# Performance work log

Measured on AMD Instinct MI355X. Metric: run time of the kernel, lower is better.

## Reference

```python
import jax, jax.numpy as jnp
import numpy as np

B, S, E, H = 8, 2048, 512, 8
D = E // H  # head_dim = 64


def setup_inputs() -> dict:
    key0 = jax.random.key(0)
    ks = jax.random.split(key0, 12)
    scale = 1.0 / np.sqrt(E)
    return {
        "value": jax.random.normal(ks[0], (B, S, E), jnp.float32),
        "key": jax.random.normal(ks[1], (B, S, E), jnp.float32),
        "query": jax.random.normal(ks[2], (B, S, E), jnp.float32),
        "mask": jax.random.randint(ks[3], (B, 1, 1, S), 0, 2, jnp.int32),
        "wq": jax.random.normal(ks[4], (E, E), jnp.float32) * scale,
        "bq": jnp.zeros((E,), jnp.float32),
        "wk": jax.random.normal(ks[5], (E, E), jnp.float32) * scale,
        "bk": jnp.zeros((E,), jnp.float32),
        "wv": jax.random.normal(ks[6], (E, E), jnp.float32) * scale,
        "bv": jnp.zeros((E,), jnp.float32),
        "wo": jax.random.normal(ks[7], (E, E), jnp.float32) * scale,
        "bo": jnp.zeros((E,), jnp.float32),
    }


def reference(value, key, query, mask, wq, bq, wk, bk, wv, bv, wo, bo):
    b, s, e = query.shape
    # projections
    q = (query @ wq + bq).reshape(b, s, H, D)  # (B,S,H,D)
    k = (key @ wk + bk).reshape(b, s, H, D)
    v = (value @ wv + bv).reshape(b, s, H, D)
    # scaled dot-product logits: (B,H,Sq,Sk)
    logits = jnp.einsum("bqhd,bkhd->bhqk", q, k) / jnp.sqrt(jnp.asarray(D, q.dtype))
    logits = logits + mask.astype(logits.dtype) * -1e9  # mask==1 -> blocked
    attn = jax.nn.softmax(logits, axis=-1)
    out = jnp.einsum("bhqk,bkhd->bqhd", attn, v).reshape(b, s, e)
    return out @ wo + bo
```

## Files before the change

kernel.cpp:

```cpp
#include <hip/hip_runtime.h>

#define Bz 8
#define Sz 2048
#define Ez 512
#define Hz 8
#define Dz 64

typedef _Float16 f16;
typedef __attribute__((ext_vector_type(2))) _Float16 f16x2;
typedef __attribute__((ext_vector_type(8))) _Float16 f16x8;
typedef __attribute__((ext_vector_type(4))) float f32x4;

#define LOG2E 1.44269504f

__device__ __forceinline__ void async16(const void* g, void* l) {
    __builtin_amdgcn_global_load_lds(
        (const __attribute__((address_space(1))) unsigned int*)g,
        (__attribute__((address_space(3))) unsigned int*)l, 16, 0, 0);
}

__device__ __forceinline__ f16x2 pkrtz(float a, float b) {
    return __builtin_bit_cast(f16x2, __builtin_amdgcn_cvt_pkrtz(a, b));
}

__device__ __forceinline__ int swz(int row) {
    return (row & 7) ^ ((2 * ((row >> 3) & 3)) & 7);
}

__global__ __launch_bounds__(256)
void cast_kernel(const float* __restrict__ q, const float* __restrict__ k,
                 const float* __restrict__ v, const int* __restrict__ mask,
                 f16* __restrict__ qa, f16* __restrict__ ka, f16* __restrict__ va,
                 int* __restrict__ rnk, int* __restrict__ slen)
{
    const int z = blockIdx.y;
    const int tid = threadIdx.x;
    if (z == 3) {
        const int b = blockIdx.x;
        if (b >= Bz) return;
        __shared__ int sc2[2][256];
        const int* mp = mask + (size_t)b * Sz;
        int m[8], c = 0;
        #pragma unroll
        for (int j = 0; j < 8; ++j) { m[j] = mp[tid*8 + j]; c += (m[j] == 0); }
        sc2[0][tid] = c;
        __syncthreads();
        int src = 0;
        #pragma unroll
        for (int s = 1; s < 256; s <<= 1) {
            int vv = sc2[src][tid] + ((tid >= s) ? sc2[src][tid - s] : 0);
            sc2[src ^ 1][tid] = vv;
            src ^= 1;
            __syncthreads();
        }
        int incl = sc2[src][tid];
        int base = incl - c;
        if (tid == 255) slen[b] = incl;
        int kk = base;
        int r8[8];
        #pragma unroll
        for (int j = 0; j < 8; ++j) {
            r8[j] = (m[j] == 0) ? kk : -1;
            kk += (m[j] == 0);
        }
        #pragma unroll
        for (int j = 0; j < 8; ++j) rnk[(size_t)b * Sz + tid*8 + j] = r8[j];
        return;
    }
    const int i = blockIdx.x * 256 + tid;
    const float* src = (z == 0) ? q : (z == 1) ? k : v;
    f16* dst = (z == 0) ? qa : (z == 1) ? ka : va;
    float4 x = *(const float4*)&src[(size_t)i * 4];
    f16x2 h0 = pkrtz(x.x, x.y), h1 = pkrtz(x.z, x.w);
    f16 h[4] = {h0[0], h0[1], h1[0], h1[1]};
    *(uint2*)&dst[(size_t)i * 4] = *(uint2*)h;
}

__global__ __launch_bounds__(256)
void prep_w(const float* __restrict__ W0, const float* __restrict__ W1,
            const float* __restrict__ W2, const float* __restrict__ W3,
            f16* __restrict__ T0, f16* __restrict__ T1,
            f16* __restrict__ T2, f16* __restrict__ T3)
{
    __shared__ float S[64][68];
    const float* W = (blockIdx.z==0)?W0:(blockIdx.z==1)?W1:(blockIdx.z==2)?W2:W3;
    f16*         T = (blockIdx.z==0)?T0:(blockIdx.z==1)?T1:(blockIdx.z==2)?T2:T3;
    const float sc = (blockIdx.z == 0) ? 0.125f * LOG2E : 1.0f;
    const int k0 = blockIdx.x * 64, n0 = blockIdx.y * 64;
    const int tid = threadIdx.x;
    {
        int kr = tid >> 4, nc = (tid & 15) * 4;
        #pragma unroll
        for (int i = 0; i < 4; ++i) {
            float4 w4 = *(const float4*)&W[(size_t)(k0 + kr + i*16) * Ez + n0 + nc];
            S[kr + i*16][nc+0] = w4.x; S[kr + i*16][nc+1] = w4.y;
            S[kr + i*16][nc+2] = w4.z; S[kr + i*16][nc+3] = w4.w;
        }
    }
    __syncthreads();
    {
        int n = tid >> 2, kq = tid & 3;
        f16 h[16];
        #pragma unroll
        for (int j = 0; j < 16; ++j) h[j] = (f16)(S[kq*16 + j][n] * sc);
        f16* dst = &T[(size_t)(n0 + n) * Ez + k0 + kq*16];
        *(uint4*)&dst[0] = *(uint4*)&h[0];
        *(uint4*)&dst[8] = *(uint4*)&h[8];
    }
}

__global__ __launch_bounds__(256)
void compact_v(const f16* __restrict__ vp, const int* __restrict__ slen,
               f16* __restrict__ vt)
{
    const int ct = blockIdx.x, h = blockIdx.y, b = blockIdx.z;
    const int sl = slen[b];
    if (ct * 64 >= sl && !(ct == 0 && sl == 0)) return;
    __shared__ f16 S[64 * 72];
    const int tid = threadIdx.x;
    {
        int r = tid >> 2, ch = tid & 3;
        int j = ct * 64 + r;
        uint4 v0 = {0,0,0,0}, v1 = {0,0,0,0};
        if (j < sl) {
            const f16* srcp = vp + (((size_t)b * Hz + h) * Sz + j) * Dz + ch * 16;
            v0 = *(const uint4*)&srcp[0];
            v1 = *(const uint4*)&srcp[8];
        }
        *(uint4*)&S[r*72 + ch*16]     = v0;
        *(uint4*)&S[r*72 + ch*16 + 8] = v1;
    }
    __syncthreads();
    {
        int d = tid >> 2, kq = tid & 3;
        f16 hh[16];
        #pragma unroll
        for (int j = 0; j < 16; ++j) hh[j] = S[(kq*16 + j)*72 + d];
        f16* dst = vt + (((size_t)b * Hz + h) * Dz + d) * Sz + ct*64 + kq*16;
        *(uint4*)&dst[0] = *(uint4*)&hh[0];
        *(uint4*)&dst[8] = *(uint4*)&hh[8];
    }
}

__global__ __launch_bounds__(256, 4)
void proj_gemm(const f16* __restrict__ qa, const f16* __restrict__ ka,
               const f16* __restrict__ va,
               const f16* __restrict__ wtq, const f16* __restrict__ wtk,
               const f16* __restrict__ wtv,
               const float* __restrict__ bqp, const float* __restrict__ bkp,
               const float* __restrict__ bvp, const int* __restrict__ rnk,
               f16* __restrict__ qp, f16* __restrict__ kp, f16* __restrict__ vp)
{
    __shared__ __align__(16) char lds[32768];
    const int z = blockIdx.z;
    const f16* A  = (z==0)?qa:(z==1)?ka:va;
    const f16* Wt = (z==0)?wtq:(z==1)?wtk:wtv;
    const float* bias = (z==0)?bqp:(z==1)?bkp:bvp;
    f16* C16 = (z==0)?qp:(z==1)?kp:vp;
    const float bscale = (z==0) ? 0.125f*LOG2E : 1.0f;

    const int tid  = threadIdx.x;
    const int lane = tid & 63, w = tid >> 6;
    const int col  = lane & 15, quad = lane >> 4;
    const int wm = w & 1, wn = w >> 1;
    const int m0 = blockIdx.x * 128, n0 = blockIdx.y * 128;
    const int srow = lane >> 2, schunk = lane & 3;

    f32x4 acc[4][4];
    #pragma unroll
    for (int i = 0; i < 4; ++i)
        #pragma unroll
        for (int j = 0; j < 4; ++j) acc[i][j] = (f32x4){0.f,0.f,0.f,0.f};

    auto issue = [&](int t, int buf) {
        f16* As = (f16*)(lds + buf * 16384);
        f16* Ws = As + 4096;
        #pragma unroll
        for (int i = 0; i < 2; ++i) {
            int row = w*32 + i*16 + srow;
            int cl = schunk ^ ((row >> 1) & 3);
            async16(&A[(size_t)(m0 + row) * Ez + t*32 + cl*8],  &As[row*32 + schunk*8]);
            async16(&Wt[(size_t)(n0 + row) * Ez + t*32 + cl*8], &Ws[row*32 + schunk*8]);
        }
    };

    issue(0, 0);
    const int xrc = (col >> 1) & 3;

    for (int t = 0; t < 16; ++t) {
        const int cur = t & 1;
        __syncthreads();
        if (t < 15) issue(t + 1, cur ^ 1);
        f16* As = (f16*)(lds + cur * 16384);
        f16* Ws = As + 4096;
        f16x8 af[4];
        #pragma unroll
        for (int mi = 0; mi < 4; ++mi)
            af[mi] = *(const f16x8*)&As[(wm*64 + mi*16 + col)*32 + ((quad ^ xrc)*8)];
        #pragma unroll
        for (int ni = 0; ni < 4; ++ni) {
            f16x8 wf = *(const f16x8*)&Ws[(wn*64 + ni*16 + col)*32 + ((quad ^ xrc)*8)];
            #pragma unroll
            for (int mi = 0; mi < 4; ++mi)
                acc[mi][ni] = __builtin_amdgcn_mfma_f32_16x16x32_f16(af[mi], wf, acc[mi][ni], 0,0,0);
        }
    }

    const int rw = tid >> 1, half = tid & 1;
    const int m = m0 + rw, b = m >> 11, s = m & (Sz-1);
    int rowout = s;
    bool dostore = true;
    if (z != 0) {
        int rk = rnk[(size_t)b * Sz + s];
        dostore = (rk >= 0);
        rowout = rk;
    }

    f16* Tr = (f16*)lds;
    #pragma unroll
    for (int p = 0; p < 2; ++p) {
        __syncthreads();
        if (wn == p) {
            #pragma unroll
            for (int ni = 0; ni < 4; ++ni) {
                float bv = bias[n0 + p*64 + ni*16 + col] * bscale;
                #pragma unroll
                for (int mi = 0; mi < 4; ++mi)
                    #pragma unroll
                    for (int rr = 0; rr < 4; ++rr) {
                        int ml = wm*64 + mi*16 + quad*4 + rr;
                        Tr[ml*72 + ni*16 + col] = (f16)(acc[mi][ni][rr] + bv);
                    }
            }
        }
        __syncthreads();
        if (dostore) {
            int hh = (n0 >> 6) + p;
            f16* dst = &C16[(((size_t)b*Hz + hh)*Sz + rowout)*Dz + half*32];
            const f16* srcp = &Tr[rw*72 + half*32];
            #pragma unroll
            for (int j = 0; j < 4; ++j)
                *(uint4*)&dst[j*8] = *(const uint4*)&srcp[j*8];
        }
    }
}

__global__ __launch_bounds__(256, 4)
void out_gemm(const f16* __restrict__ A, const f16* __restrict__ Wt,
              const float* __restrict__ bias, float* __restrict__ Cf)
{
    __shared__ __align__(16) char lds[32768];
    const int tid  = threadIdx.x;
    const int lane = tid & 63, w = tid >> 6;
    const int col  = lane & 15, quad = lane >> 4;
    const int wm = w & 1, wn = w >> 1;
    const int m0 = blockIdx.x * 128, n0 = blockIdx.y * 128;
    const int srow = lane >> 2, schunk = lane & 3;

    f32x4 acc[4][4];
    #pragma unroll
    for (int i = 0; i < 4; ++i)
        #pragma unroll
        for (int j = 0; j < 4; ++j) acc[i][j] = (f32x4){0.f,0.f,0.f,0.f};

    auto issue = [&](int t, int buf) {
        f16* As = (f16*)(lds + buf * 16384);
        f16* Ws = As + 4096;
        #pragma unroll
        for (int i = 0; i < 2; ++i) {
            int row = w*32 + i*16 + srow;
            int cl = schunk ^ ((row >> 1) & 3);
            async16(&A[(size_t)(m0 + row) * Ez + t*32 + cl*8],  &As[row*32 + schunk*8]);
            async16(&Wt[(size_t)(n0 + row) * Ez + t*32 + cl*8], &Ws[row*32 + schunk*8]);
        }
    };

    issue(0, 0);
    const int xrc = (col >> 1) & 3;

    for (int t = 0; t < 16; ++t) {
        const int cur = t & 1;
        __syncthreads();
        if (t < 15) issue(t + 1, cur ^ 1);
        f16* As = (f16*)(lds + cur * 16384);
        f16* Ws = As + 4096;
        f16x8 af[4];
        #pragma unroll
        for (int mi = 0; mi < 4; ++mi)
            af[mi] = *(const f16x8*)&As[(wm*64 + mi*16 + col)*32 + ((quad ^ xrc)*8)];
        #pragma unroll
        for (int ni = 0; ni < 4; ++ni) {
            f16x8 wf = *(const f16x8*)&Ws[(wn*64 + ni*16 + col)*32 + ((quad ^ xrc)*8)];
            #pragma unroll
            for (int mi = 0; mi < 4; ++mi)
                acc[mi][ni] = __builtin_amdgcn_mfma_f32_16x16x32_f16(af[mi], wf, acc[mi][ni], 0,0,0);
        }
    }

    #pragma unroll
    for (int ni = 0; ni < 4; ++ni) {
        int n = n0 + wn*64 + ni*16 + col;
        float bv = bias[n];
        #pragma unroll
        for (int mi = 0; mi < 4; ++mi)
            #pragma unroll
            for (int rr = 0; rr < 4; ++rr) {
                int m = m0 + wm*64 + mi*16 + quad*4 + rr;
                Cf[(size_t)m * Ez + n] = acc[mi][ni][rr] + bv;
            }
    }
}

__global__ __launch_bounds__(256, 4)
void attn_f16(const f16* __restrict__ Q, const f16* __restrict__ K,
              const f16* __restrict__ VT, const int* __restrict__ slen,
              f16* __restrict__ O)
{
    __shared__ __align__(16) f16 KS[2][64*64];
    __shared__ __align__(16) f16 VS[2][64*64];

    const int tid  = threadIdx.x;
    const int lane = tid & 63, w = tid >> 6;
    const int col  = lane & 15, quad = lane >> 4;

    const int blk = blockIdx.x;
    const int xcd = blk & 7, slot = blk >> 3;
    const int bh = xcd + 8 * (slot >> 4);
    const int qb = slot & 15;
    const int b = bh >> 3, h = bh & 7;

    const int sl = slen[b];
    int nt = (sl + 63) >> 6;
    if (nt < 1) nt = 1;

    const int q0 = qb * 128 + w * 32;

    f16x8 qf[2][2];
    #pragma unroll
    for (int qt = 0; qt < 2; ++qt)
        #pragma unroll
        for (int ks = 0; ks < 2; ++ks)
            qf[qt][ks] = *(const f16x8*)&Q[((size_t)bh*Sz + q0 + qt*16 + col)*Dz + ks*32 + quad*8];

    const f16* Kp = K + (size_t)bh * Sz * Dz;
    const f16* Vp = VT + (size_t)bh * Dz * Sz;

    const int srow = lane >> 3, sch = lane & 7;
    const int row0 = w*16 + srow, row1 = row0 + 8;
    const int cl0 = sch ^ swz(row0), cl1 = sch ^ swz(row1);

    int keyrow[4], gk[4];
    #pragma unroll
    for (int kc = 0; kc < 4; ++kc) {
        keyrow[kc] = 32*(kc>>1) + 8*(col>>2) + 4*(kc&1) + (col&3);
        gk[kc] = swz(keyrow[kc]);
    }

    f32x4 oacc[2][4];
    #pragma unroll
    for (int qt = 0; qt < 2; ++qt)
        #pragma unroll
        for (int dc = 0; dc < 4; ++dc) oacc[qt][dc] = (f32x4){0.f,0.f,0.f,0.f};
    const f32x4 zero4 = (f32x4){0.f, 0.f, 0.f, 0.f};
    f32x4 lacc[2] = {(f32x4){0.f,0.f,0.f,0.f}, (f32x4){0.f,0.f,0.f,0.f}};
    f16x8 one8;
    #pragma unroll
    for (int i = 0; i < 8; ++i) one8[i] = (f16)1.0f;

    auto issue = [&](int t, int buf) {
        async16(&Kp[(size_t)(t*64 + row0)*Dz + cl0*8], &KS[buf][row0*64 + sch*8]);
        async16(&Vp[(size_t)row0*Sz + t*64 + cl0*8],   &VS[buf][row0*64 + sch*8]);
        async16(&Kp[(size_t)(t*64 + row1)*Dz + cl1*8], &KS[buf][row1*64 + sch*8]);
        async16(&Vp[(size_t)row1*Sz + t*64 + cl1*8],   &VS[buf][row1*64 + sch*8]);
    };

    issue(0, 0);

    for (int t = 0; t < nt; ++t) {
        const int cur = t & 1;
        __syncthreads();
        if (t + 1 < nt) issue(t + 1, cur ^ 1);

        f32x4 sc[2][4];
        __builtin_amdgcn_s_setprio(1);
        #pragma unroll
        for (int kc = 0; kc < 4; ++kc) {
            f16x8 kf0 = *(const f16x8*)&KS[cur][keyrow[kc]*64 + ((quad ^ gk[kc])*8)];
            f16x8 kf1 = *(const f16x8*)&KS[cur][keyrow[kc]*64 + (((4 + quad) ^ gk[kc])*8)];
            sc[0][kc] = __builtin_amdgcn_mfma_f32_16x16x32_f16(kf0, qf[0][0], zero4, 0,0,0);
            sc[1][kc] = __builtin_amdgcn_mfma_f32_16x16x32_f16(kf0, qf[1][0], zero4, 0,0,0);
            sc[0][kc] = __builtin_amdgcn_mfma_f32_16x16x32_f16(kf1, qf[0][1], sc[0][kc], 0,0,0);
            sc[1][kc] = __builtin_amdgcn_mfma_f32_16x16x32_f16(kf1, qf[1][1], sc[1][kc], 0,0,0);
        }
        __builtin_amdgcn_s_setprio(0);

        const bool last = (t == nt - 1);
        union { f16x2 h2[4]; f16x8 h8; } ph[2][2];
        #pragma unroll
        for (int qt = 0; qt < 2; ++qt) {
            #pragma unroll
            for (int kg = 0; kg < 2; ++kg) {
                float e0 = __builtin_amdgcn_exp2f(sc[qt][2*kg][0]);
                float e1 = __builtin_amdgcn_exp2f(sc[qt][2*kg][1]);
                float e2 = __builtin_amdgcn_exp2f(sc[qt][2*kg][2]);
                float e3 = __builtin_amdgcn_exp2f(sc[qt][2*kg][3]);
                float e4 = __builtin_amdgcn_exp2f(sc[qt][2*kg+1][0]);
                float e5 = __builtin_amdgcn_exp2f(sc[qt][2*kg+1][1]);
                float e6 = __builtin_amdgcn_exp2f(sc[qt][2*kg+1][2]);
                float e7 = __builtin_amdgcn_exp2f(sc[qt][2*kg+1][3]);
                if (last) {
                    int rem = sl - t*64 - 32*kg - 8*quad;
                    e0 = (rem > 0) ? e0 : 0.f; e1 = (rem > 1) ? e1 : 0.f;
                    e2 = (rem > 2) ? e2 : 0.f; e3 = (rem > 3) ? e3 : 0.f;
                    e4 = (rem > 4) ? e4 : 0.f; e5 = (rem > 5) ? e5 : 0.f;
                    e6 = (rem > 6) ? e6 : 0.f; e7 = (rem > 7) ? e7 : 0.f;
                }
                ph[qt][kg].h2[0] = pkrtz(e0, e1);
                ph[qt][kg].h2[1] = pkrtz(e2, e3);
                ph[qt][kg].h2[2] = pkrtz(e4, e5);
                ph[qt][kg].h2[3] = pkrtz(e6, e7);
            }
        }

        __builtin_amdgcn_s_setprio(1);
        lacc[0] = __builtin_amdgcn_mfma_f32_16x16x32_f16(one8, ph[0][0].h8, lacc[0], 0,0,0);
        lacc[1] = __builtin_amdgcn_mfma_f32_16x16x32_f16(one8, ph[1][0].h8, lacc[1], 0,0,0);
        lacc[0] = __builtin_amdgcn_mfma_f32_16x16x32_f16(one8, ph[0][1].h8, lacc[0], 0,0,0);
        lacc[1] = __builtin_amdgcn_mfma_f32_16x16x32_f16(one8, ph[1][1].h8, lacc[1], 0,0,0);
        #pragma unroll
        for (int dc = 0; dc < 4; ++dc) {
            const int d = dc*16 + col;
            const int gd = swz(d);
            #pragma unroll
            for (int kg = 0; kg < 2; ++kg) {
                f16x8 vf = *(const f16x8*)&VS[cur][d*64 + (((kg*4 + quad) ^ gd)*8)];
                oacc[0][dc] = __builtin_amdgcn_mfma_f32_16x16x32_f16(vf, ph[0][kg].h8, oacc[0][dc], 0,0,0);
                oacc[1][dc] = __builtin_amdgcn_mfma_f32_16x16x32_f16(vf, ph[1][kg].h8, oacc[1][dc], 0,0,0);
            }
        }
        __builtin_amdgcn_s_setprio(0);
    }

    float inv[2];
    inv[0] = 1.0f / lacc[0][0];
    inv[1] = 1.0f / lacc[1][0];
    #pragma unroll
    for (int qt = 0; qt < 2; ++qt) {
        const int q = q0 + qt*16 + col;
        f16* op = &O[((size_t)b*Sz + q)*Ez + h*Dz];
        #pragma unroll
        for (int dc = 0; dc < 4; ++dc) {
            f16 ov[4] = {(f16)(oacc[qt][dc][0]*inv[qt]), (f16)(oacc[qt][dc][1]*inv[qt]),
                         (f16)(oacc[qt][dc][2]*inv[qt]), (f16)(oacc[qt][dc][3]*inv[qt])};
            *(uint2*)&op[dc*16 + quad*4] = *(uint2*)ov;
        }
    }
}

extern "C" void kernel_launch(void* const* d_in, const int* in_sizes, int n_in,
                              void* d_out, int out_size, void* d_ws, size_t ws_size,
                              hipStream_t stream)
{
    const float* value = (const float*)d_in[0];
    const float* key   = (const float*)d_in[1];
    const float* query = (const float*)d_in[2];
    const int*   mask  = (const int*)d_in[3];
    const float* wq = (const float*)d_in[4];
    const float* bq = (const float*)d_in[5];
    const float* wk = (const float*)d_in[6];
    const float* bk = (const float*)d_in[7];
    const float* wv = (const float*)d_in[8];
    const float* bv = (const float*)d_in[9];
    const float* wo = (const float*)d_in[10];
    const float* bo = (const float*)d_in[11];
    float* out = (float*)d_out;

    const size_t nW   = (size_t)Ez * Ez;
    const size_t nAct = (size_t)Bz * Sz * Ez;
    f16* wtq = (f16*)d_ws;
    f16* wtk = wtq + nW;
    f16* wtv = wtk + nW;
    f16* wto = wtv + nW;
    f16* qa  = wto + nW;
    f16* ka  = qa + nAct;
    f16* va  = ka + nAct;
    f16* qp  = va + nAct;
    f16* kp  = qp + nAct;
    f16* vp  = kp + nAct;
    f16* vt  = vp + nAct;
    f16* o16 = vt + nAct;
    int* rnkp = (int*)(o16 + nAct);
    int* slenp = rnkp + Bz * Sz;

    cast_kernel<<<dim3(8192, 4), 256, 0, stream>>>(query, key, value, mask,
                                                   qa, ka, va, rnkp, slenp);
    prep_w<<<dim3(8, 8, 4), 256, 0, stream>>>(wq, wk, wv, wo, wtq, wtk, wtv, wto);

    proj_gemm<<<dim3(128, 4, 3), 256, 0, stream>>>(qa, ka, va, wtq, wtk, wtv,
                                                   bq, bk, bv, rnkp, qp, kp, vp);

    compact_v<<<dim3(32, Hz, Bz), 256, 0, stream>>>(vp, slenp, vt);

    attn_f16<<<1024, 256, 0, stream>>>(qp, kp, vt, slenp, o16);

    out_gemm<<<dim3(128, 4), 256, 0, stream>>>(o16, wto, bo, out);
}
```

Before: 273.3 us.

## Fuse V compaction and transpose into projection GEMM epilogue

Removes the separate compact_v kernel. The V projection epilogue now scatters unmasked rows straight into the transposed, compacted vt layout, using an LDS rank-to-row map and a per-tile minimum rank. The tail padding up to a multiple of 64 is zeroed in the mask-scan block of cast_kernel. This saves one launch and one full round trip of V through memory, but the transposed stores are 2-byte strided writes, which may coalesce poorly.

Result: no change. 278.0 us (+1.7%).

```diff
diff --git a/kernel.cpp b/kernel.cpp
--- a/kernel.cpp
+++ b/kernel.cpp
@@ -31,7 +31,7 @@
 void cast_kernel(const float* __restrict__ q, const float* __restrict__ k,
                  const float* __restrict__ v, const int* __restrict__ mask,
                  f16* __restrict__ qa, f16* __restrict__ ka, f16* __restrict__ va,
-                 int* __restrict__ rnk, int* __restrict__ slen)
+                 int* __restrict__ rnk, int* __restrict__ slen, f16* __restrict__ vt)
 {
     const int z = blockIdx.y;
     const int tid = threadIdx.x;
@@ -39,6 +39,7 @@
         const int b = blockIdx.x;
         if (b >= Bz) return;
         __shared__ int sc2[2][256];
+        __shared__ int ssl;
         const int* mp = mask + (size_t)b * Sz;
         int m[8], c = 0;
         #pragma unroll
@@ -55,7 +56,7 @@
         }
         int incl = sc2[src][tid];
         int base = incl - c;
-        if (tid == 255) slen[b] = incl;
+        if (tid == 255) { slen[b] = incl; ssl = incl; }
         int kk = base;
         int r8[8];
         #pragma unroll
@@ -65,6 +66,15 @@
         }
         #pragma unroll
         for (int j = 0; j < 8; ++j) rnk[(size_t)b * Sz + tid*8 + j] = r8[j];
+        __syncthreads();
+        const int sl2 = ssl;
+        const int pad = (sl2 + 63) & ~63;
+        if (pad > sl2) {
+            for (int pr = tid; pr < Hz * Dz; pr += 256) {
+                f16* dst = vt + ((size_t)b * Hz * Dz + pr) * Sz;
+                for (int j = sl2; j < pad; ++j) dst[j] = (f16)0.f;
+            }
+        }
         return;
     }
     const int i = blockIdx.x * 256 + tid;
@@ -109,39 +119,6 @@
     }
 }
 
-__global__ __launch_bounds__(256)
-void compact_v(const f16* __restrict__ vp, const int* __restrict__ slen,
-               f16* __restrict__ vt)
-{
-    const int ct = blockIdx.x, h = blockIdx.y, b = blockIdx.z;
-    const int sl = slen[b];
-    if (ct * 64 >= sl && !(ct == 0 && sl == 0)) return;
-    __shared__ f16 S[64 * 72];
-    const int tid = threadIdx.x;
-    {
-        int r = tid >> 2, ch = tid & 3;
-        int j = ct * 64 + r;
-        uint4 v0 = {0,0,0,0}, v1 = {0,0,0,0};
-        if (j < sl) {
-            const f16* srcp = vp + (((size_t)b * Hz + h) * Sz + j) * Dz + ch * 16;
-            v0 = *(const uint4*)&srcp[0];
-            v1 = *(const uint4*)&srcp[8];
-        }
-        *(uint4*)&S[r*72 + ch*16]     = v0;
-        *(uint4*)&S[r*72 + ch*16 + 8] = v1;
-    }
-    __syncthreads();
-    {
-        int d = tid >> 2, kq = tid & 3;
-        f16 hh[16];
-        #pragma unroll
-        for (int j = 0; j < 16; ++j) hh[j] = S[(kq*16 + j)*72 + d];
-        f16* dst = vt + (((size_t)b * Hz + h) * Dz + d) * Sz + ct*64 + kq*16;
-        *(uint4*)&dst[0] = *(uint4*)&hh[0];
-        *(uint4*)&dst[8] = *(uint4*)&hh[8];
-    }
-}
-
 __global__ __launch_bounds__(256, 4)
 void proj_gemm(const f16* __restrict__ qa, const f16* __restrict__ ka,
                const f16* __restrict__ va,
@@ -149,14 +126,13 @@
                const f16* __restrict__ wtv,
                const float* __restrict__ bqp, const float* __restrict__ bkp,
                const float* __restrict__ bvp, const int* __restrict__ rnk,
-               f16* __restrict__ qp, f16* __restrict__ kp, f16* __restrict__ vp)
+               f16* __restrict__ qp, f16* __restrict__ kp, f16* __restrict__ vt)
 {
     __shared__ __align__(16) char lds[32768];
     const int z = blockIdx.z;
     const f16* A  = (z==0)?qa:(z==1)?ka:va;
     const f16* Wt = (z==0)?wtq:(z==1)?wtk:wtv;
     const float* bias = (z==0)?bqp:(z==1)?bkp:bvp;
-    f16* C16 = (z==0)?qp:(z==1)?kp:vp;
     const float bscale = (z==0) ? 0.125f*LOG2E : 1.0f;
 
     const int tid  = threadIdx.x;
@@ -206,12 +182,37 @@
         }
     }
 
+    const int bb = m0 >> 11;
+    const int TS = (z == 2) ? 73 : 72;
+
+    int* rks  = (int*)(lds + 20480);
+    int* clp  = (int*)(lds + 22528);
+    int* sr0p = (int*)(lds + 24576);
+    int r0v = 0x7fffffff;
+    if (z == 2) {
+        __syncthreads();
+        if (tid == 0) sr0p[0] = 0x7fffffff;
+        if (tid < 128) clp[tid] = -1;
+        __syncthreads();
+        if (tid < 128) {
+            int rb = rnk[(size_t)bb * Sz + ((m0 + tid) & (Sz - 1))];
+            rks[tid] = rb;
+            if (rb >= 0) atomicMin(sr0p, rb);
+        }
+        __syncthreads();
+        r0v = sr0p[0];
+        if (tid < 128) {
+            int rb = rks[tid];
+            if (rb >= 0) clp[rb - r0v] = tid;
+        }
+    }
+
     const int rw = tid >> 1, half = tid & 1;
-    const int m = m0 + rw, b = m >> 11, s = m & (Sz-1);
+    const int s = (m0 + rw) & (Sz - 1);
     int rowout = s;
     bool dostore = true;
-    if (z != 0) {
-        int rk = rnk[(size_t)b * Sz + s];
+    if (z == 1) {
+        int rk = rnk[(size_t)bb * Sz + s];
         dostore = (rk >= 0);
         rowout = rk;
     }
@@ -229,18 +230,34 @@
                     #pragma unroll
                     for (int rr = 0; rr < 4; ++rr) {
                         int ml = wm*64 + mi*16 + quad*4 + rr;
-                        Tr[ml*72 + ni*16 + col] = (f16)(acc[mi][ni][rr] + bv);
+                        Tr[ml*TS + ni*16 + col] = (f16)(acc[mi][ni][rr] + bv);
                     }
             }
         }
         __syncthreads();
-        if (dostore) {
-            int hh = (n0 >> 6) + p;
-            f16* dst = &C16[(((size_t)b*Hz + hh)*Sz + rowout)*Dz + half*32];
-            const f16* srcp = &Tr[rw*72 + half*32];
-            #pragma unroll
-            for (int j = 0; j < 4; ++j)
-                *(uint4*)&dst[j*8] = *(const uint4*)&srcp[j*8];
+        const int hh = (n0 >> 6) + p;
+        if (z != 2) {
+            if (dostore) {
+                f16* C16 = (z == 0) ? qp : kp;
+                f16* dst = &C16[(((size_t)bb*Hz + hh)*Sz + rowout)*Dz + half*32];
+                const f16* srcp = &Tr[rw*TS + half*32];
+                #pragma unroll
+                for (int j = 0; j < 4; ++j)
+                    *(uint4*)&dst[j*8] = *(const uint4*)&srcp[j*8];
+            }
+        } else if (r0v != 0x7fffffff) {
+            const int jlane = tid & 63, dgrp = tid >> 6;
+            #pragma unroll
+            for (int dd = 0; dd < 16; ++dd) {
+                const int d = dgrp * 16 + dd;
+                f16* dstb = vt + (((size_t)bb * Hz + hh) * Dz + d) * Sz + r0v;
+                #pragma unroll
+                for (int jh = 0; jh < 2; ++jh) {
+                    const int j = jh * 64 + jlane;
+                    const int sr = clp[j];
+                    if (sr >= 0) dstb[j] = Tr[sr * 73 + d];
+                }
+            }
         }
     }
 }
@@ -486,20 +503,17 @@
     f16* va  = ka + nAct;
     f16* qp  = va + nAct;
     f16* kp  = qp + nAct;
-    f16* vp  = kp + nAct;
-    f16* vt  = vp + nAct;
+    f16* vt  = kp + nAct;
     f16* o16 = vt + nAct;
     int* rnkp = (int*)(o16 + nAct);
     int* slenp = rnkp + Bz * Sz;
 
     cast_kernel<<<dim3(8192, 4), 256, 0, stream>>>(query, key, value, mask,
-                                                   qa, ka, va, rnkp, slenp);
+                                                   qa, ka, va, rnkp, slenp, vt);
     prep_w<<<dim3(8, 8, 4), 256, 0, stream>>>(wq, wk, wv, wo, wtq, wtk, wtv, wto);
 
     proj_gemm<<<dim3(128, 4, 3), 256, 0, stream>>>(qa, ka, va, wtq, wtk, wtv,
-                                                   bq, bk, bv, rnkp, qp, kp, vp);
-
-    compact_v<<<dim3(32, Hz, Bz), 256, 0, stream>>>(vp, slenp, vt);
+                                                   bq, bk, bv, rnkp, qp, kp, vt);
 
     attn_f16<<<1024, 256, 0, stream>>>(qp, kp, vt, slenp, o16);
 
```
